# Performance work log

Hardware: AMD Instinct MI355X
Metric: run time of the kernel (lower is better)

Reference implementation:

```python
import jax, jax.numpy as jnp
import numpy as np

B, L, D = 16, 2048, 128
GROUP = 16
NG = L // GROUP  # number of groups per batch
ALPHA = 0.5


def setup_inputs() -> dict:
    key = jax.random.key(0)
    k0, k1, k2 = jax.random.split(key, 3)
    x = jax.random.normal(k0, (B, L, D), dtype=jnp.float32)
    # per-batch permutation = gather indices (each position used exactly once)
    group_tensor = jax.vmap(lambda k: jax.random.permutation(k, L))(
        jax.random.split(k1, B)).astype(jnp.int32)
    ctxlens = jnp.full((B,), L, dtype=jnp.int32)
    W = jax.random.normal(k2, (2 * D,), dtype=jnp.float32) * (1.0 / np.sqrt(D))
    norm_alpha = jnp.ones((2,), dtype=jnp.float32)
    norm_gamma = jnp.ones((2 * D,), dtype=jnp.float32)
    norm_beta = jnp.zeros((2 * D,), dtype=jnp.float32)
    return {"x": x, "group_tensor": group_tensor, "ctxlens": ctxlens, "W": W,
            "norm_alpha": norm_alpha, "norm_gamma": norm_gamma, "norm_beta": norm_beta}


def _leaky_relu(v):
    return jnp.where(v >= 0, v, 0.01 * v)


def _ncn_forward(x, group_tensor, ctxlens, W, norm_alpha, norm_gamma, norm_beta):
    Bd, Ld, Dd = x.shape
    ng = Ld // GROUP
    Wi, Wj = W[:Dd], W[Dd:]
    a1, a2 = norm_alpha[0], norm_alpha[1]
    g1, g2 = norm_gamma[:Dd], norm_gamma[Dd:]
    b1, b2 = norm_beta[:Dd], norm_beta[Dd:]

    # gather x by group indices -> [B, NG, GROUP, D]
    xg = jnp.take_along_axis(x, group_tensor[:, :, None].astype(jnp.int32), axis=1)
    xg = xg.reshape(Bd, ng, GROUP, Dd)

    def step(carry, j):
        xi, xa = carry  # each [B, NG, GROUP, D]
        xj = jax.lax.dynamic_slice_in_dim(xi, j, 1, axis=2)  # [B, NG, 1, D]
        sim = jnp.einsum('bgnd,d->bgn', xi, Wi) \
            + jnp.einsum('bgd,d->bg', xj[:, :, 0, :], Wj)[:, :, None]  # [B,NG,GROUP]
        T = ALPHA * xi + (1.0 - ALPHA) * sim[..., None] * xj
        T_norm = g1 * jnp.tanh(a1 * T) + b1
        Fv = _leaky_relu(T_norm)
        xa = xa + Fv                               # ya = xa + F
        xi = xi + g2 * jnp.tanh(a2 * xa) + b2      # yi = xi + norm2(ya)
        return (xi, xa), None

    (yi, ya), _ = jax.lax.scan(step, (xg, jnp.zeros_like(xg)), jnp.arange(GROUP))

    # kernel only processes/stores a group if its start offset < ctxlen
    valid = (jnp.arange(ng, dtype=jnp.int32) * GROUP)[None, :] < ctxlens[:, None]
    yi = jnp.where(valid[:, :, None, None], yi, 0.0).reshape(Bd, Ld, Dd)
    ya = jnp.where(valid[:, :, None, None], ya, 0.0).reshape(Bd, Ld, Dd)

    # scatter back to original positions
    bidx = jnp.arange(Bd)[:, None]
    yi_out = jnp.zeros_like(x).at[bidx, group_tensor].set(yi)
    ya_out = jnp.zeros_like(x).at[bidx, group_tensor].set(ya)
    return yi_out, ya_out


def reference(x, group_tensor, ctxlens, W, norm_alpha, norm_gamma, norm_beta):
    return _ncn_forward(x, group_tensor, ctxlens, W, norm_alpha, norm_gamma, norm_beta)
```

## Files before the change

### kernel.cpp

```cpp
#include <hip/hip_runtime.h>

#define B_ 16
#define L_ 2048
#define D_ 128
#define GROUP_ 16
#define NG_ (L_ / GROUP_)
#define LOG2E_ 1.44269504088896340736f

typedef float v2 __attribute__((ext_vector_type(2)));

template<int CTRL>
__device__ __forceinline__ float dpp_add(float v) {
    int x = __builtin_amdgcn_update_dpp(0, __float_as_int(v), CTRL, 0xF, 0xF, false);
    return v + __int_as_float(x);
}
__device__ __forceinline__ float row16_sum(float v) {
    v = dpp_add<0xB1>(v);
    v = dpp_add<0x4E>(v);
    v = dpp_add<0x141>(v);
    v = dpp_add<0x140>(v);
    return v;
}

#define LGKM_BARRIER() asm volatile("s_waitcnt lgkmcnt(0)\n\ts_barrier" ::: "memory")

#define STEP_LOOP(SELFN)                                                      \
    for (int j = 0; j < GROUP_; ++j) {                                        \
        const int p = j & 1;                                                  \
        v2 xjv[4];                                                            \
        {                                                                     \
            float4 tA = *(const float4*)&s_xj[p][d0];                         \
            float4 tB = *(const float4*)&s_xj[p][d0 + 4];                     \
            xjv[0] = (v2){tA.x, tA.y}; xjv[1] = (v2){tA.z, tA.w};             \
            xjv[2] = (v2){tB.x, tB.y}; xjv[3] = (v2){tB.z, tB.w};             \
        }                                                                     \
        v2 sv = (v2){0.0f, 0.0f};                                             \
        _Pragma("unroll")                                                     \
        for (int k = 0; k < 4; ++k) sv = __builtin_elementwise_fma(cxi[k], Wi[k], sv); \
        _Pragma("unroll")                                                     \
        for (int k = 0; k < 4; ++k) sv = __builtin_elementwise_fma(xjv[k], Wj[k], sv); \
        const float sim = row16_sum(sv.x + sv.y);                             \
        const v2 simv = (v2){sim, sim};                                       \
        _Pragma("unroll")                                                     \
        for (int k = 0; k < 4; ++k) {                                         \
            v2 u  = __builtin_elementwise_fma(simv, xjv[k], cxi[k]);          \
            v2 r1 = (v2){__builtin_amdgcn_rcpf(__builtin_amdgcn_exp2f(u.x) + 1.0f),   \
                         __builtin_amdgcn_rcpf(__builtin_amdgcn_exp2f(u.y) + 1.0f)};  \
            v2 tnS = __builtin_elementwise_fma(G1S[k], r1, B1S[k]);           \
            v2 FvS = SELFN(tnS, tnS * leak);                                  \
            za[k] += FvS;                                                     \
            v2 r2 = (v2){__builtin_amdgcn_rcpf(__builtin_amdgcn_exp2f(za[k].x) + 1.0f), \
                         __builtin_amdgcn_rcpf(__builtin_amdgcn_exp2f(za[k].y) + 1.0f)}; \
            cxi[k] = __builtin_elementwise_fma(G2c[k], r2, cxi[k] + B2c[k]);  \
        }                                                                     \
        if (j + 1 < GROUP_ && row == j + 1) {                                 \
            float4 oA = {cxi[0].x, cxi[0].y, cxi[1].x, cxi[1].y};             \
            float4 oB = {cxi[2].x, cxi[2].y, cxi[3].x, cxi[3].y};             \
            *(float4*)&s_xj[p ^ 1][d0]     = oA;                              \
            *(float4*)&s_xj[p ^ 1][d0 + 4] = oB;                              \
        }                                                                     \
        LGKM_BARRIER();                                                       \
    }

__global__ __launch_bounds__(256)
__attribute__((amdgpu_waves_per_eu(4, 4)))
void ncn_kernel(
    const float* __restrict__ x,
    const int*   __restrict__ gt,
    const int*   __restrict__ ctxlens,
    const float* __restrict__ W,
    const float* __restrict__ nalpha,
    const float* __restrict__ ngamma,
    const float* __restrict__ nbeta,
    float* __restrict__ out)
{
    const int blk = blockIdx.x;
    const int b   = blk >> 7;
    const int g   = blk & (NG_ - 1);
    const int tid = threadIdx.x;
    const int row = tid >> 4;
    const int rl  = tid & 15;
    const int d0  = rl << 3;

    __shared__ float s_xj[2][D_];

    const float a1 = nalpha[0];
    const float a2 = nalpha[1];
    const float ca = -a1 * LOG2E_;
    const float S  = -2.0f * a2 * LOG2E_;
    const float inv_ca = 1.0f / ca;
    const bool  selMin = (S < 0.0f);

    v2 Wi[4], Wj[4], G1S[4], B1S[4], G2c[4], B2c[4];
    {
        float4 wA = *(const float4*)(W + d0);
        float4 wB = *(const float4*)(W + d0 + 4);
        float4 vA = *(const float4*)(W + D_ + d0);
        float4 vB = *(const float4*)(W + D_ + d0 + 4);
        Wi[0] = inv_ca * (v2){wA.x, wA.y}; Wi[1] = inv_ca * (v2){wA.z, wA.w};
        Wi[2] = inv_ca * (v2){wB.x, wB.y}; Wi[3] = inv_ca * (v2){wB.z, wB.w};
        Wj[0] = inv_ca * (v2){vA.x, vA.y}; Wj[1] = inv_ca * (v2){vA.z, vA.w};
        Wj[2] = inv_ca * (v2){vB.x, vB.y}; Wj[3] = inv_ca * (v2){vB.z, vB.w};

        float4 g1A = *(const float4*)(ngamma + d0);
        float4 g1B = *(const float4*)(ngamma + d0 + 4);
        float4 g2A = *(const float4*)(ngamma + D_ + d0);
        float4 g2B = *(const float4*)(ngamma + D_ + d0 + 4);
        float4 b1A = *(const float4*)(nbeta + d0);
        float4 b1B = *(const float4*)(nbeta + d0 + 4);
        float4 b2A = *(const float4*)(nbeta + D_ + d0);
        float4 b2B = *(const float4*)(nbeta + D_ + d0 + 4);

        v2 g1v[4] = {(v2){g1A.x,g1A.y},(v2){g1A.z,g1A.w},(v2){g1B.x,g1B.y},(v2){g1B.z,g1B.w}};
        v2 b1v[4] = {(v2){b1A.x,b1A.y},(v2){b1A.z,b1A.w},(v2){b1B.x,b1B.y},(v2){b1B.z,b1B.w}};
        v2 g2v[4] = {(v2){g2A.x,g2A.y},(v2){g2A.z,g2A.w},(v2){g2B.x,g2B.y},(v2){g2B.z,g2B.w}};
        v2 b2v[4] = {(v2){b2A.x,b2A.y},(v2){b2A.z,b2A.w},(v2){b2B.x,b2B.y},(v2){b2B.z,b2B.w}};
#pragma unroll
        for (int k = 0; k < 4; ++k) {
            G1S[k] = (S * 2.0f) * g1v[k];
            B1S[k] = S * (b1v[k] - g1v[k]);
            G2c[k] = (ca * 2.0f) * g2v[k];
            B2c[k] = ca * (b2v[k] - g2v[k]);
        }
    }

    const int l   = g * GROUP_ + row;
    const int tok = gt[b * L_ + l];
    const float* xp = x + ((size_t)(b * L_ + tok)) * D_ + d0;

    v2 cxi[4], za[4];
    {
        float4 xA = *(const float4*)xp;
        float4 xB = *(const float4*)(xp + 4);
        const v2 cav = (v2){ca, ca};
        cxi[0] = cav * (v2){xA.x, xA.y}; cxi[1] = cav * (v2){xA.z, xA.w};
        cxi[2] = cav * (v2){xB.x, xB.y}; cxi[3] = cav * (v2){xB.z, xB.w};
    }
#pragma unroll
    for (int k = 0; k < 4; ++k) za[k] = (v2){0.0f, 0.0f};

    if (row == 0) {
        float4 oA = {cxi[0].x, cxi[0].y, cxi[1].x, cxi[1].y};
        float4 oB = {cxi[2].x, cxi[2].y, cxi[3].x, cxi[3].y};
        *(float4*)&s_xj[0][d0]     = oA;
        *(float4*)&s_xj[0][d0 + 4] = oB;
    }
    __syncthreads();

    const v2 leak = (v2){0.01f, 0.01f};

    if (selMin) {
        STEP_LOOP(__builtin_elementwise_min)
    } else {
        STEP_LOOP(__builtin_elementwise_max)
    }

    const float invS = 1.0f / S;
    const v2 invSv  = (v2){invS, invS};
    const v2 invCav = (v2){inv_ca, inv_ca};
    v2 xi[4], xa[4];
#pragma unroll
    for (int k = 0; k < 4; ++k) {
        xi[k] = cxi[k] * invCav;
        xa[k] = za[k] * invSv;
    }

    const bool valid = (g * GROUP_) < ctxlens[b];
    if (!valid) {
#pragma unroll
        for (int k = 0; k < 4; ++k) { xi[k] = (v2){0,0}; xa[k] = (v2){0,0}; }
    }

    float* o1 = out + ((size_t)(b * L_ + tok)) * D_ + d0;
    float* o2 = o1 + (size_t)B_ * L_ * D_;
    float4 s1A = {xi[0].x, xi[0].y, xi[1].x, xi[1].y};
    float4 s1B = {xi[2].x, xi[2].y, xi[3].x, xi[3].y};
    float4 s2A = {xa[0].x, xa[0].y, xa[1].x, xa[1].y};
    float4 s2B = {xa[2].x, xa[2].y, xa[3].x, xa[3].y};
    *(float4*)o1       = s1A;
    *(float4*)(o1 + 4) = s1B;
    *(float4*)o2       = s2A;
    *(float4*)(o2 + 4) = s2B;
}

extern "C" void kernel_launch(void* const* d_in, const int* in_sizes, int n_in,
                              void* d_out, int out_size, void* d_ws, size_t ws_size,
                              hipStream_t stream) {
    const float* x  = (const float*)d_in[0];
    const int*   gt = (const int*)d_in[1];
    const int*   cl = (const int*)d_in[2];
    const float* W  = (const float*)d_in[3];
    const float* na = (const float*)d_in[4];
    const float* ng = (const float*)d_in[5];
    const float* nb = (const float*)d_in[6];
    float* out = (float*)d_out;

    ncn_kernel<<<B_ * NG_, 256, 0, stream>>>(x, gt, cl, W, na, ng, nb, out);
}
```

Baseline: 111.1 us.

## Process two group rows per thread with 128-thread blocks

Each thread now handles two rows of a group (rows r and r+8), so a block shrinks from 256 to 128 threads (two waves instead of four). The xj·Wj projection is computed once per step and shared by both rows, and the two independent row updates give more instruction-level parallelism between barriers. The cost is higher register pressure and fewer waves per block to hide the latency of the transcendental ops.

```diff
diff --git a/kernel.cpp b/kernel.cpp
--- a/kernel.cpp
+++ b/kernel.cpp
@@ -23,6 +23,20 @@
 }
 
 #define LGKM_BARRIER() asm volatile("s_waitcnt lgkmcnt(0)\n\ts_barrier" ::: "memory")
+
+#define UPDATE_ROW(CXI, ZA, SIMV, SELFN)                                      \
+    _Pragma("unroll")                                                         \
+    for (int k = 0; k < 4; ++k) {                                             \
+        v2 u  = __builtin_elementwise_fma(SIMV, xjv[k], CXI[k]);              \
+        v2 r1 = (v2){__builtin_amdgcn_rcpf(__builtin_amdgcn_exp2f(u.x) + 1.0f),   \
+                     __builtin_amdgcn_rcpf(__builtin_amdgcn_exp2f(u.y) + 1.0f)};  \
+        v2 tnS = __builtin_elementwise_fma(G1S[k], r1, B1S[k]);               \
+        v2 FvS = SELFN(tnS, tnS * leak);                                      \
+        ZA[k] += FvS;                                                         \
+        v2 r2 = (v2){__builtin_amdgcn_rcpf(__builtin_amdgcn_exp2f(ZA[k].x) + 1.0f), \
+                     __builtin_amdgcn_rcpf(__builtin_amdgcn_exp2f(ZA[k].y) + 1.0f)}; \
+        CXI[k] = __builtin_elementwise_fma(G2c[k], r2, CXI[k] + B2c[k]);      \
+    }
 
 #define STEP_LOOP(SELFN)                                                      \
     for (int j = 0; j < GROUP_; ++j) {                                        \
@@ -34,35 +48,39 @@
             xjv[0] = (v2){tA.x, tA.y}; xjv[1] = (v2){tA.z, tA.w};             \
             xjv[2] = (v2){tB.x, tB.y}; xjv[3] = (v2){tB.z, tB.w};             \
         }                                                                     \
-        v2 sv = (v2){0.0f, 0.0f};                                             \
+                            \
+        v2 pjv = (v2){0.0f, 0.0f};                                            \
         _Pragma("unroll")                                                     \
-        for (int k = 0; k < 4; ++k) sv = __builtin_elementwise_fma(cxi[k], Wi[k], sv); \
+        for (int k = 0; k < 4; ++k) pjv = __builtin_elementwise_fma(xjv[k], Wj[k], pjv); \
+        v2 svA = pjv, svB = pjv;                                              \
         _Pragma("unroll")                                                     \
-        for (int k = 0; k < 4; ++k) sv = __builtin_elementwise_fma(xjv[k], Wj[k], sv); \
-        const float sim = row16_sum(sv.x + sv.y);                             \
-        const v2 simv = (v2){sim, sim};                                       \
+        for (int k = 0; k < 4; ++k) svA = __builtin_elementwise_fma(cxiA[k], Wi[k], svA); \
         _Pragma("unroll")                                                     \
-        for (int k = 0; k < 4; ++k) {                                         \
-            v2 u  = __builtin_elementwise_fma(simv, xjv[k], cxi[k]);          \
-            v2 r1 = (v2){__builtin_amdgcn_rcpf(__builtin_amdgcn_exp2f(u.x) + 1.0f),   \
-                         __builtin_amdgcn_rcpf(__builtin_amdgcn_exp2f(u.y) + 1.0f)};  \
-            v2 tnS = __builtin_elementwise_fma(G1S[k], r1, B1S[k]);           \
-            v2 FvS = SELFN(tnS, tnS * leak);                                  \
-            za[k] += FvS;                                                     \
-            v2 r2 = (v2){__builtin_amdgcn_rcpf(__builtin_amdgcn_exp2f(za[k].x) + 1.0f), \
-                         __builtin_amdgcn_rcpf(__builtin_amdgcn_exp2f(za[k].y) + 1.0f)}; \
-            cxi[k] = __builtin_elementwise_fma(G2c[k], r2, cxi[k] + B2c[k]);  \
-        }                                                                     \
-        if (j + 1 < GROUP_ && row == j + 1) {                                 \
-            float4 oA = {cxi[0].x, cxi[0].y, cxi[1].x, cxi[1].y};             \
-            float4 oB = {cxi[2].x, cxi[2].y, cxi[3].x, cxi[3].y};             \
-            *(float4*)&s_xj[p ^ 1][d0]     = oA;                              \
-            *(float4*)&s_xj[p ^ 1][d0 + 4] = oB;                              \
+        for (int k = 0; k < 4; ++k) svB = __builtin_elementwise_fma(cxiB[k], Wi[k], svB); \
+        const float simA = row16_sum(svA.x + svA.y);                          \
+        const float simB = row16_sum(svB.x + svB.y);                          \
+        const v2 simAv = (v2){simA, simA};                                    \
+        const v2 simBv = (v2){simB, simB};                                    \
+        UPDATE_ROW(cxiA, zaA, simAv, SELFN)                                   \
+        UPDATE_ROW(cxiB, zaB, simBv, SELFN)                                   \
+        const int jn = j + 1;                                                 \
+        if (jn < GROUP_ && rp == (jn & 7)) {                                  \
+            if (jn & 8) {                                                     \
+                float4 oA = {cxiB[0].x, cxiB[0].y, cxiB[1].x, cxiB[1].y};     \
+                float4 oB = {cxiB[2].x, cxiB[2].y, cxiB[3].x, cxiB[3].y};     \
+                *(float4*)&s_xj[p ^ 1][d0]     = oA;                          \
+                *(float4*)&s_xj[p ^ 1][d0 + 4] = oB;                          \
+            } else {                                                          \
+                float4 oA = {cxiA[0].x, cxiA[0].y, cxiA[1].x, cxiA[1].y};     \
+                float4 oB = {cxiA[2].x, cxiA[2].y, cxiA[3].x, cxiA[3].y};     \
+                *(float4*)&s_xj[p ^ 1][d0]     = oA;                          \
+                *(float4*)&s_xj[p ^ 1][d0 + 4] = oB;                          \
+            }                                                                 \
         }                                                                     \
         LGKM_BARRIER();                                                       \
     }
 
-__global__ __launch_bounds__(256)
+__global__ __launch_bounds__(128)
 __attribute__((amdgpu_waves_per_eu(4, 4)))
 void ncn_kernel(
     const float* __restrict__ x,
@@ -78,7 +96,7 @@
     const int b   = blk >> 7;
     const int g   = blk & (NG_ - 1);
     const int tid = threadIdx.x;
-    const int row = tid >> 4;
+    const int rp  = tid >> 4;
     const int rl  = tid & 15;
     const int d0  = rl << 3;
 
@@ -124,24 +142,30 @@
         }
     }
 
-    const int l   = g * GROUP_ + row;
-    const int tok = gt[b * L_ + l];
-    const float* xp = x + ((size_t)(b * L_ + tok)) * D_ + d0;
-
-    v2 cxi[4], za[4];
+    const int lA   = g * GROUP_ + rp;
+    const int tokA = gt[b * L_ + lA];
+    const int tokB = gt[b * L_ + lA + 8];
+    const float* xpA = x + ((size_t)(b * L_ + tokA)) * D_ + d0;
+    const float* xpB = x + ((size_t)(b * L_ + tokB)) * D_ + d0;
+
+    v2 cxiA[4], zaA[4], cxiB[4], zaB[4];
     {
-        float4 xA = *(const float4*)xp;
-        float4 xB = *(const float4*)(xp + 4);
         const v2 cav = (v2){ca, ca};
-        cxi[0] = cav * (v2){xA.x, xA.y}; cxi[1] = cav * (v2){xA.z, xA.w};
-        cxi[2] = cav * (v2){xB.x, xB.y}; cxi[3] = cav * (v2){xB.z, xB.w};
-    }
-#pragma unroll
-    for (int k = 0; k < 4; ++k) za[k] = (v2){0.0f, 0.0f};
-
-    if (row == 0) {
-        float4 oA = {cxi[0].x, cxi[0].y, cxi[1].x, cxi[1].y};
-        float4 oB = {cxi[2].x, cxi[2].y, cxi[3].x, cxi[3].y};
+        float4 xA = *(const float4*)xpA;
+        float4 xB = *(const float4*)(xpA + 4);
+        cxiA[0] = cav * (v2){xA.x, xA.y}; cxiA[1] = cav * (v2){xA.z, xA.w};
+        cxiA[2] = cav * (v2){xB.x, xB.y}; cxiA[3] = cav * (v2){xB.z, xB.w};
+        float4 yA = *(const float4*)xpB;
+        float4 yB = *(const float4*)(xpB + 4);
+        cxiB[0] = cav * (v2){yA.x, yA.y}; cxiB[1] = cav * (v2){yA.z, yA.w};
+        cxiB[2] = cav * (v2){yB.x, yB.y}; cxiB[3] = cav * (v2){yB.z, yB.w};
+    }
+#pragma unroll
+    for (int k = 0; k < 4; ++k) { zaA[k] = (v2){0.0f, 0.0f}; zaB[k] = (v2){0.0f, 0.0f}; }
+
+    if (rp == 0) {
+        float4 oA = {cxiA[0].x, cxiA[0].y, cxiA[1].x, cxiA[1].y};
+        float4 oB = {cxiA[2].x, cxiA[2].y, cxiA[3].x, cxiA[3].y};
         *(float4*)&s_xj[0][d0]     = oA;
         *(float4*)&s_xj[0][d0 + 4] = oB;
     }
@@ -158,29 +182,45 @@
     const float invS = 1.0f / S;
     const v2 invSv  = (v2){invS, invS};
     const v2 invCav = (v2){inv_ca, inv_ca};
-    v2 xi[4], xa[4];
+
+    const bool valid = (g * GROUP_) < ctxlens[b];
+
+    float* o1A = out + ((size_t)(b * L_ + tokA)) * D_ + d0;
+    float* o1B = out + ((size_t)(b * L_ + tokB)) * D_ + d0;
+    float* o2A = o1A + (size_t)B_ * L_ * D_;
+    float* o2B = o1B + (size_t)B_ * L_ * D_;
+
+    v2 yiA[4], yaA[4], yiB[4], yaB[4];
 #pragma unroll
     for (int k = 0; k < 4; ++k) {
-        xi[k] = cxi[k] * invCav;
-        xa[k] = za[k] * invSv;
-    }
-
-    const bool valid = (g * GROUP_) < ctxlens[b];
+        yiA[k] = cxiA[k] * invCav; yaA[k] = zaA[k] * invSv;
+        yiB[k] = cxiB[k] * invCav; yaB[k] = zaB[k] * invSv;
+    }
     if (!valid) {
 #pragma unroll
-        for (int k = 0; k < 4; ++k) { xi[k] = (v2){0,0}; xa[k] = (v2){0,0}; }
-    }
-
-    float* o1 = out + ((size_t)(b * L_ + tok)) * D_ + d0;
-    float* o2 = o1 + (size_t)B_ * L_ * D_;
-    float4 s1A = {xi[0].x, xi[0].y, xi[1].x, xi[1].y};
-    float4 s1B = {xi[2].x, xi[2].y, xi[3].x, xi[3].y};
-    float4 s2A = {xa[0].x, xa[0].y, xa[1].x, xa[1].y};
-    float4 s2B = {xa[2].x, xa[2].y, xa[3].x, xa[3].y};
-    *(float4*)o1       = s1A;
-    *(float4*)(o1 + 4) = s1B;
-    *(float4*)o2       = s2A;
-    *(float4*)(o2 + 4) = s2B;
+        for (int k = 0; k < 4; ++k) {
+            yiA[k] = (v2){0,0}; yaA[k] = (v2){0,0};
+            yiB[k] = (v2){0,0}; yaB[k] = (v2){0,0};
+        }
+    }
+
+    float4 s1A = {yiA[0].x, yiA[0].y, yiA[1].x, yiA[1].y};
+    float4 s1B = {yiA[2].x, yiA[2].y, yiA[3].x, yiA[3].y};
+    float4 s2A = {yaA[0].x, yaA[0].y, yaA[1].x, yaA[1].y};
+    float4 s2B = {yaA[2].x, yaA[2].y, yaA[3].x, yaA[3].y};
+    *(float4*)o1A       = s1A;
+    *(float4*)(o1A + 4) = s1B;
+    *(float4*)o2A       = s2A;
+    *(float4*)(o2A + 4) = s2B;
+
+    float4 t1A = {yiB[0].x, yiB[0].y, yiB[1].x, yiB[1].y};
+    float4 t1B = {yiB[2].x, yiB[2].y, yiB[3].x, yiB[3].y};
+    float4 t2A = {yaB[0].x, yaB[0].y, yaB[1].x, yaB[1].y};
+    float4 t2B = {yaB[2].x, yaB[2].y, yaB[3].x, yaB[3].y};
+    *(float4*)o1B       = t1A;
+    *(float4*)(o1B + 4) = t1B;
+    *(float4*)o2B       = t2A;
+    *(float4*)(o2B + 4) = t2B;
 }
 
 extern "C" void kernel_launch(void* const* d_in, const int* in_sizes, int n_in,
@@ -195,5 +235,5 @@
     const float* nb = (const float*)d_in[6];
     float* out = (float*)d_out;
 
-    ncn_kernel<<<B_ * NG_, 256, 0, stream>>>(x, gt, cl, W, na, ng, nb, out);
-}
+    ncn_kernel<<<B_ * NG_, 128, 0, stream>>>(x, gt, cl, W, na, ng, nb, out);
+}
```

Result: no change. 112.6 us (+1.4%).
